# Kernel optimization log

Measured on AMD Instinct MI355X. Metric: run time of the kernel, lower is better.

The kernel has to match this reference:

```python
import jax, jax.numpy as jnp
import numpy as np
import math

B, N = 1, 768
C1, C2 = 384, 128
H, SQK, SV, PQK, PV, NC = 12, 16, 16, 4, 8, 384
EPS = 1e-8
SCALAR_W = math.sqrt(1.0 / (3.0 * SQK))           # sqrt(1/(num_logit_terms*scalar_variance))
POINT_W = math.sqrt(1.0 / (3.0 * (PQK * 9.0 / 2.0)))
W2D = math.sqrt(1.0 / 3.0)


def _quat_to_rot(q):
    # q: [..., 4] -> orthonormal rotation matrices [..., 3, 3]
    q = q / jnp.linalg.norm(q, axis=-1, keepdims=True)
    w, x, y, z = q[..., 0], q[..., 1], q[..., 2], q[..., 3]
    r0 = jnp.stack([1 - 2 * (y * y + z * z), 2 * (x * y - w * z), 2 * (x * z + w * y)], -1)
    r1 = jnp.stack([2 * (x * y + w * z), 1 - 2 * (x * x + z * z), 2 * (y * z - w * x)], -1)
    r2 = jnp.stack([2 * (x * z - w * y), 2 * (y * z + w * x), 1 - 2 * (x * x + y * y)], -1)
    return jnp.stack([r0, r1, r2], -2)


def setup_inputs() -> dict:
    key = jax.random.key(0)
    ks = jax.random.split(key, 12)

    def lin(k, o, i):
        kw, kb = jax.random.split(k)
        w = jax.random.normal(kw, (o, i), jnp.float32) / np.sqrt(i).astype(np.float32)
        b = jax.random.normal(kb, (o,), jnp.float32) * 0.01
        return w, b

    w_qs, b_qs = lin(ks[0], H * SQK, C1)
    w_kvs, b_kvs = lin(ks[1], H * (SV + SQK), C1)
    w_qp, b_qp = lin(ks[2], H * 3 * PQK, C1)
    w_kvp, b_kvp = lin(ks[3], H * 3 * (PQK + PV), C1)
    w_a2, b_a2 = lin(ks[4], H, C2)
    w_o, b_o = lin(ks[5], NC, H * (C2 + SV + 4 * PV))
    return {
        'inputs_1d': jax.random.normal(ks[6], (B, N, C1), jnp.float32),
        'inputs_2d': jax.random.normal(ks[7], (B, N, N, C2), jnp.float32),
        'mask': jnp.ones((B, N, 1), jnp.float32),
        'rotation': _quat_to_rot(jax.random.normal(ks[8], (B, N, 4), jnp.float32)),
        'translation': jax.random.normal(ks[9], (B, N, 3), jnp.float32) * 10.0,
        'w_q_scalar': w_qs, 'b_q_scalar': b_qs,
        'w_kv_scalar': w_kvs, 'b_kv_scalar': b_kvs,
        'w_q_point': w_qp, 'b_q_point': b_qp,
        'w_kv_point': w_kvp, 'b_kv_point': b_kvp,
        'tpw': jnp.ones((H,), jnp.float32),
        'w_attn2d': w_a2, 'b_attn2d': b_a2,
        'w_out': w_o, 'b_out': b_o,
    }


def ipa_forward(inputs_1d, inputs_2d, mask, rotation, translation,
                w_q_scalar, b_q_scalar, w_kv_scalar, b_kv_scalar,
                w_q_point, b_q_point, w_kv_point, b_kv_point,
                tpw, w_attn2d, b_attn2d, w_out, b_out):
    Bs, Ns, _ = inputs_1d.shape

    # scalar q/k/v
    q_scalar = (inputs_1d @ w_q_scalar.T + b_q_scalar).reshape(Bs, Ns, H, SQK)
    kv_scalar = (inputs_1d @ w_kv_scalar.T + b_kv_scalar).reshape(Bs, Ns, H, SQK + SV)
    k_scalar, v_scalar = kv_scalar[..., :SQK], kv_scalar[..., SQK:]

    # point q/k/v in local frame; split order is 3 coord chunks of size H*P
    qp = (inputs_1d @ w_q_point.T + b_q_point).reshape(Bs, Ns, 3, H * PQK)
    kvp = (inputs_1d @ w_kv_point.T + b_kv_point).reshape(Bs, Ns, 3, H * (PQK + PV))
    # to global frame: p_global = R @ p_local + t
    qg = jnp.einsum('bnij,bnjm->bnim', rotation, qp) + translation[..., None]
    kvg = jnp.einsum('bnij,bnjm->bnim', rotation, kvp) + translation[..., None]
    q_point = qg.reshape(Bs, Ns, 3, H, PQK).transpose(0, 3, 1, 4, 2)          # [B,H,N,Pqk,3]
    kv_point = kvg.reshape(Bs, Ns, 3, H, PQK + PV).transpose(0, 3, 1, 4, 2)    # [B,H,N,Pqk+Pv,3]
    k_point, v_point = kv_point[..., :PQK, :], kv_point[..., PQK:, :]

    # point-distance attention term: sum_{p,c} (q-k)^2 = |q|^2 + |k|^2 - 2 q.k
    pw = jax.nn.softplus(tpw) * POINT_W                                       # [H]
    qn = jnp.sum(q_point * q_point, axis=(-1, -2))                             # [B,H,N]
    kn = jnp.sum(k_point * k_point, axis=(-1, -2))
    qk = jnp.einsum('bhipc,bhjpc->bhij', q_point, k_point)
    dist2 = qn[..., :, None] + kn[..., None, :] - 2.0 * qk                     # [B,H,N,N]
    attn_qk_point = -0.5 * pw[None, :, None, None] * dist2

    # scalar attention term
    attn_qk_scalar = jnp.einsum('bihd,bjhd->bhij', SCALAR_W * q_scalar, k_scalar)

    # pair-bias term
    a2d = inputs_2d @ w_attn2d.T + b_attn2d                                    # [B,N,N,H]
    logits = attn_qk_scalar + attn_qk_point + W2D * a2d.transpose(0, 3, 1, 2)

    mask2d = mask * jnp.swapaxes(mask, -1, -2)                                 # [B,N,N]
    logits = logits - 1e5 * (1.0 - mask2d[:, None, :, :])
    attn = jax.nn.softmax(logits, axis=-1)                                     # [B,H,N,N]

    # scalar values
    result_scalar = jnp.einsum('bhij,bjhd->bihd', attn, v_scalar).reshape(Bs, Ns, H * SV)

    # point values (global), then back to local frame: p_local = R^T (p - t)
    rpg = jnp.einsum('bhij,bhjpc->bhipc', attn, v_point)                       # [B,H,N,Pv,3]
    rpg = rpg.transpose(0, 2, 4, 1, 3).reshape(Bs, Ns, 3, H * PV)              # [B,N,3,M]
    local = jnp.einsum('bnji,bnjm->bnim', rotation, rpg - translation[..., None])
    dist = jnp.sqrt(EPS + jnp.sum(local * local, axis=2))                      # [B,N,M]

    # attention over pair features
    r2d = jnp.einsum('bhij,bijc->bihc', attn, inputs_2d).reshape(Bs, Ns, H * C2)

    final_act = jnp.concatenate(
        [result_scalar, local[:, :, 0], local[:, :, 1], local[:, :, 2], dist, r2d], axis=-1)
    return final_act @ w_out.T + b_out


def reference(inputs_1d, inputs_2d, mask, rotation, translation,
              w_q_scalar, b_q_scalar, w_kv_scalar, b_kv_scalar,
              w_q_point, b_q_point, w_kv_point, b_kv_point,
              tpw, w_attn2d, b_attn2d, w_out, b_out):
    return ipa_forward(inputs_1d, inputs_2d, mask, rotation, translation,
                       w_q_scalar, b_q_scalar, w_kv_scalar, b_kv_scalar,
                       w_q_point, b_q_point, w_kv_point, b_kv_point,
                       tpw, w_attn2d, b_attn2d, w_out, b_out)
```

## Files before the change

### kernel.cpp

```cpp
#include <hip/hip_runtime.h>
#include <hip/hip_bf16.h>
#include <math.h>

#define NRES 768
#define C1 384
#define C2 128
#define NH 12

#define OFF_QS   0
#define OFF_KS   147456
#define OFF_VS   294912
#define OFF_QPT  442368
#define OFF_KPT  552960
#define OFF_VPT  663552
#define OFF_FA   884736
#define OFF_RAW  OFF_FA

__device__ __forceinline__ float dot4(float4 a, float4 b) {
    return fmaf(a.x, b.x, fmaf(a.y, b.y, fmaf(a.z, b.z, a.w * b.w)));
}

static constexpr float SCALAR_W = 0.14433756729740643f;
static constexpr float POINT_W  = 0.13608276348795434f;
static constexpr float W2D_W    = 0.57735026918962576f;

__device__ __forceinline__ void wsel(int o,
    const float* w_qs, const float* b_qs, const float* w_kvs, const float* b_kvs,
    const float* w_qp, const float* b_qp, const float* w_kvp, const float* b_kvp,
    const float** row, float* bias)
{
    if (o < 192)      { *row = w_qs  + (size_t)o * C1;         *bias = b_qs[o]; }
    else if (o < 576) { *row = w_kvs + (size_t)(o - 192) * C1; *bias = b_kvs[o - 192]; }
    else if (o < 720) { *row = w_qp  + (size_t)(o - 576) * C1; *bias = b_qp[o - 576]; }
    else              { *row = w_kvp + (size_t)(o - 720) * C1; *bias = b_kvp[o - 720]; }
}

__global__ __launch_bounds__(256) void k1_gemm(
    const float* __restrict__ in1d,
    const float* __restrict__ w_qs, const float* __restrict__ b_qs,
    const float* __restrict__ w_kvs, const float* __restrict__ b_kvs,
    const float* __restrict__ w_qp, const float* __restrict__ b_qp,
    const float* __restrict__ w_kvp, const float* __restrict__ b_kvp,
    float* __restrict__ ws)
{
    __shared__ __align__(16) float ASt[32][68];
    __shared__ __align__(16) float WSt[32][68];
    const int t = threadIdx.x;
    const int n0 = blockIdx.x * 64;
    const int o0 = blockIdx.y * 64;
    const int tx = t & 15, ty = t >> 4;
    float acc[4][4];
    #pragma unroll
    for (int r = 0; r < 4; ++r)
        #pragma unroll
        for (int c = 0; c < 4; ++c) acc[r][c] = 0.f;

    for (int k0 = 0; k0 < C1; k0 += 32) {
        __syncthreads();
        #pragma unroll
        for (int s = 0; s < 2; ++s) {
            int q = t + 256 * s;
            int row = q >> 3, kq = (q & 7) * 4;
            float4 a4 = *(const float4*)&in1d[(size_t)(n0 + row) * C1 + k0 + kq];
            ASt[kq + 0][row] = a4.x; ASt[kq + 1][row] = a4.y;
            ASt[kq + 2][row] = a4.z; ASt[kq + 3][row] = a4.w;
            const float* wr; float bb;
            wsel(o0 + row, w_qs, b_qs, w_kvs, b_kvs, w_qp, b_qp, w_kvp, b_kvp, &wr, &bb);
            float4 w4 = *(const float4*)&wr[k0 + kq];
            WSt[kq + 0][row] = w4.x; WSt[kq + 1][row] = w4.y;
            WSt[kq + 2][row] = w4.z; WSt[kq + 3][row] = w4.w;
        }
        __syncthreads();
        #pragma unroll
        for (int k = 0; k < 32; ++k) {
            float4 a4 = *(const float4*)&ASt[k][ty * 4];
            float4 w4 = *(const float4*)&WSt[k][tx * 4];
            float av[4] = {a4.x, a4.y, a4.z, a4.w};
            float wv[4] = {w4.x, w4.y, w4.z, w4.w};
            #pragma unroll
            for (int r = 0; r < 4; ++r)
                #pragma unroll
                for (int c = 0; c < 4; ++c)
                    acc[r][c] = fmaf(av[r], wv[c], acc[r][c]);
        }
    }
    float bias[4];
    #pragma unroll
    for (int c = 0; c < 4; ++c) {
        const float* dummy;
        wsel(o0 + tx * 4 + c, w_qs, b_qs, w_kvs, b_kvs, w_qp, b_qp, w_kvp, b_kvp, &dummy, &bias[c]);
    }
    float* raw = ws + OFF_RAW;
    #pragma unroll
    for (int r = 0; r < 4; ++r) {
        int n = n0 + ty * 4 + r;
        *(float4*)&raw[(size_t)n * 1152 + o0 + tx * 4] =
            make_float4(acc[r][0] + bias[0], acc[r][1] + bias[1],
                        acc[r][2] + bias[2], acc[r][3] + bias[3]);
    }
}

__global__ __launch_bounds__(256) void k1b_scatter(
    const float* __restrict__ rot, const float* __restrict__ trans,
    float* __restrict__ ws)
{
    __shared__ __align__(16) float rawS[1152];
    const int t = threadIdx.x;
    const int i = blockIdx.x;
    const float* raw = ws + OFF_RAW + (size_t)i * 1152;
    for (int q = t; q < 288; q += 256) *(float4*)&rawS[q * 4] = *(const float4*)&raw[q * 4];
    __syncthreads();
    float* qs  = ws + OFF_QS;  float* ks  = ws + OFF_KS;  float* vs  = ws + OFF_VS;
    float* qpt = ws + OFF_QPT; float* kpt = ws + OFF_KPT; float* vpt = ws + OFF_VPT;

    for (int o = t; o < 576; o += 256) {
        float v = rawS[o];
        if (o < 192) {
            qs[(size_t)i * 192 + o] = v * SCALAR_W;
        } else {
            int idx = o - 192, h = idx >> 5, d = idx & 31;
            if (d < 16) ks[(size_t)i * 192 + h * 16 + d] = v;
            else        vs[(size_t)i * 192 + h * 16 + (d - 16)] = v;
        }
    }
    if (t < 192) {
        int m = t;
        float x0, x1, x2;
        if (m < 48) { x0 = rawS[576 + m]; x1 = rawS[624 + m]; x2 = rawS[672 + m]; }
        else { int mm = m - 48; x0 = rawS[720 + mm]; x1 = rawS[864 + mm]; x2 = rawS[1008 + mm]; }
        float g[3];
        #pragma unroll
        for (int ii = 0; ii < 3; ++ii)
            g[ii] = rot[i * 9 + ii * 3 + 0] * x0 + rot[i * 9 + ii * 3 + 1] * x1 +
                    rot[i * 9 + ii * 3 + 2] * x2 + trans[i * 3 + ii];
        if (m < 48) {
            #pragma unroll
            for (int ii = 0; ii < 3; ++ii) qpt[(size_t)i * 144 + 3 * m + ii] = g[ii];
        } else {
            int mm = m - 48, h = mm / 12, pp = mm % 12;
            if (pp < 4) {
                #pragma unroll
                for (int ii = 0; ii < 3; ++ii) kpt[(size_t)i * 144 + h * 12 + pp * 3 + ii] = g[ii];
            } else {
                #pragma unroll
                for (int ii = 0; ii < 3; ++ii) vpt[(size_t)i * 288 + h * 24 + (pp - 4) * 3 + ii] = g[ii];
            }
        }
    }
}

#define TJ 256
__global__ __launch_bounds__(256) void k2_attn(
    const float* __restrict__ in2d,
    const float* __restrict__ mask,
    const float* __restrict__ rot, const float* __restrict__ trans,
    const float* __restrict__ tpw,
    const float* __restrict__ w2d, const float* __restrict__ b2d,
    float* __restrict__ ws)
{
    __shared__ __align__(16) float P[NH][264];
    __shared__ __align__(16) float tileS[64][128];
    __shared__ __align__(16) float qsS[192];
    __shared__ __align__(16) float qptS[144];
    __shared__ float qnS[NH], phS[NH], bbS[NH], mS[NH], lS[NH], aS[NH];
    __shared__ float rpgS[288];
    const int t = threadIdx.x;
    const int i = blockIdx.x;

    const float* qs  = ws + OFF_QS;  const float* ks  = ws + OFF_KS;  const float* vs = ws + OFF_VS;
    const float* qpt = ws + OFF_QPT; const float* kpt = ws + OFF_KPT; const float* vpt = ws + OFF_VPT;

    if (t < 48) *(float4*)&qsS[t * 4] = *(const float4*)&qs[(size_t)i * 192 + t * 4];
    else if (t >= 64 && t < 100) { int u = t - 64; *(float4*)&qptS[u * 4] = *(const float4*)&qpt[(size_t)i * 144 + u * 4]; }
    __syncthreads();
    if (t < NH) {
        float s = 0.f;
        #pragma unroll
        for (int e = 0; e < 12; ++e) { float x = qptS[t * 12 + e]; s += x * x; }
        qnS[t] = s;
        phS[t] = -0.5f * POINT_W * logf(1.f + __expf(tpw[t]));
        bbS[t] = W2D_W * b2d[t];
        mS[t] = -1e30f;
        lS[t] = 0.f;
    }
    __syncthreads();
    const float mi = mask[i];

    float ra[4] = {0.f, 0.f, 0.f, 0.f};
    float rb[4] = {0.f, 0.f, 0.f, 0.f};
    const bool isR2 = (t < 192);
    int h0 = 0, h1 = 0, c4 = 0, o0 = 0, vh = 0;
    const float* vbase = nullptr; int vstride = 0; bool vact = false;
    if (isR2) { h0 = (t >> 5) * 2; h1 = h0 + 1; c4 = t & 31; }
    else {
        int u = t - 192; o0 = u * 8; vact = (u < 60);
        if (vact) {
            if (o0 < 192) { vh = o0 >> 4; vbase = vs + o0; vstride = 192; }
            else { int q0 = o0 - 192; vh = q0 / 24; vbase = vpt + q0; vstride = 288; }
        }
    }

    for (int tile = 0; tile < 3; ++tile) {
        const int j0 = tile * TJ;
        __syncthreads();
        {
            const int j = j0 + t;
            float acc[NH];
            #pragma unroll
            for (int h = 0; h < NH; ++h) acc[h] = 0.f;
            const float* row = in2d + ((size_t)i * NRES + j) * C2;
            #pragma unroll 8
            for (int cc = 0; cc < 32; ++cc) {
                float4 v4 = *(const float4*)&row[cc * 4];
                #pragma unroll
                for (int h = 0; h < NH; ++h) {
                    float4 w4 = *(const float4*)&w2d[h * C2 + cc * 4];
                    acc[h] += dot4(v4, w4);
                }
            }
            const float msub = -100000.0f * (1.0f - mi * mask[j]);
            const float* ksr  = ks  + (size_t)j * 192;
            const float* kptr = kpt + (size_t)j * 144;
            #pragma unroll
            for (int h = 0; h < NH; ++h) {
                float sq = 0.f;
                #pragma unroll
                for (int d4 = 0; d4 < 4; ++d4) {
                    float4 q4 = *(const float4*)&qsS[h * 16 + d4 * 4];
                    float4 k4 = *(const float4*)&ksr[h * 16 + d4 * 4];
                    sq += dot4(q4, k4);
                }
                float qk = 0.f, kk = 0.f;
                #pragma unroll
                for (int e4 = 0; e4 < 3; ++e4) {
                    float4 qp4 = *(const float4*)&qptS[h * 12 + e4 * 4];
                    float4 kp4 = *(const float4*)&kptr[h * 12 + e4 * 4];
                    qk += dot4(qp4, kp4);
                    kk += dot4(kp4, kp4);
                }
                P[h][t] = sq + phS[h] * (qnS[h] + kk - 2.f * qk) + W2D_W * acc[h] + bbS[h] + msub;
            }
        }
        __syncthreads();
        {
            int wv = t >> 6, lane = t & 63;
            for (int h = wv * 3; h < wv * 3 + 3; ++h) {
                float v0 = P[h][lane], v1 = P[h][lane + 64], v2 = P[h][lane + 128], v3 = P[h][lane + 192];
                float mt = fmaxf(fmaxf(v0, v1), fmaxf(v2, v3));
                #pragma unroll
                for (int off = 32; off > 0; off >>= 1) mt = fmaxf(mt, __shfl_xor(mt, off));
                float mold = mS[h];
                float mnew = fmaxf(mold, mt);
                float e0 = __expf(v0 - mnew), e1 = __expf(v1 - mnew);
                float e2 = __expf(v2 - mnew), e3 = __expf(v3 - mnew);
                P[h][lane] = e0; P[h][lane + 64] = e1; P[h][lane + 128] = e2; P[h][lane + 192] = e3;
                float s = e0 + e1 + e2 + e3;
                #pragma unroll
                for (int off = 32; off > 0; off >>= 1) s += __shfl_xor(s, off);
                if (lane == 0) {
                    float a = __expf(mold - mnew);
                    aS[h] = a;
                    lS[h] = lS[h] * a + s;
                    mS[h] = mnew;
                }
            }
        }
        __syncthreads();
        if (isR2) {
            float a0 = aS[h0], a1 = aS[h1];
            #pragma unroll
            for (int k = 0; k < 4; ++k) { ra[k] *= a0; rb[k] *= a1; }
        } else if (vact) {
            float a = aS[vh];
            #pragma unroll
            for (int k = 0; k < 4; ++k) { ra[k] *= a; rb[k] *= a; }
        }
        for (int sub = 0; sub < 4; ++sub) {
            __syncthreads();
            #pragma unroll
            for (int s = 0; s < 8; ++s) {
                int q = t + 256 * s;
                int rr = q >> 5, cc = q & 31;
                *(float4*)&tileS[rr][cc * 4] =
                    *(const float4*)&in2d[((size_t)i * NRES + j0 + sub * 64 + rr) * C2 + cc * 4];
            }
            __syncthreads();
            if (isR2) {
                for (int jj = 0; jj < 64; jj += 4) {
                    int jt = sub * 64 + jj;
                    float4 p0 = *(const float4*)&P[h0][jt];
                    float4 p1 = *(const float4*)&P[h1][jt];
                    float w0[4] = {p0.x, p0.y, p0.z, p0.w};
                    float w1[4] = {p1.x, p1.y, p1.z, p1.w};
                    #pragma unroll
                    for (int k = 0; k < 4; ++k) {
                        float4 v4 = *(const float4*)&tileS[jj + k][c4 * 4];
                        ra[0] = fmaf(w0[k], v4.x, ra[0]); ra[1] = fmaf(w0[k], v4.y, ra[1]);
                        ra[2] = fmaf(w0[k], v4.z, ra[2]); ra[3] = fmaf(w0[k], v4.w, ra[3]);
                        rb[0] = fmaf(w1[k], v4.x, rb[0]); rb[1] = fmaf(w1[k], v4.y, rb[1]);
                        rb[2] = fmaf(w1[k], v4.z, rb[2]); rb[3] = fmaf(w1[k], v4.w, rb[3]);
                    }
                }
            } else if (vact) {
                for (int jj = 0; jj < 64; jj += 4) {
                    int jt = sub * 64 + jj;
                    int jg = j0 + jt;
                    float4 p = *(const float4*)&P[vh][jt];
                    float w[4] = {p.x, p.y, p.z, p.w};
                    #pragma unroll
                    for (int k = 0; k < 4; ++k) {
                        float4 va = *(const float4*)&vbase[(size_t)(jg + k) * vstride];
                        float4 vb = *(const float4*)&vbase[(size_t)(jg + k) * vstride + 4];
                        ra[0] = fmaf(w[k], va.x, ra[0]); ra[1] = fmaf(w[k], va.y, ra[1]);
                        ra[2] = fmaf(w[k], va.z, ra[2]); ra[3] = fmaf(w[k], va.w, ra[3]);
                        rb[0] = fmaf(w[k], vb.x, rb[0]); rb[1] = fmaf(w[k], vb.y, rb[1]);
                        rb[2] = fmaf(w[k], vb.z, rb[2]); rb[3] = fmaf(w[k], vb.w, rb[3]);
                    }
                }
            }
        }
    }
    float* fa = ws + OFF_FA + (size_t)i * 2112;
    if (isR2) {
        float n0v = 1.f / lS[h0], n1v = 1.f / lS[h1];
        *(float4*)&fa[576 + h0 * 128 + c4 * 4] = make_float4(ra[0] * n0v, ra[1] * n0v, ra[2] * n0v, ra[3] * n0v);
        *(float4*)&fa[576 + h1 * 128 + c4 * 4] = make_float4(rb[0] * n1v, rb[1] * n1v, rb[2] * n1v, rb[3] * n1v);
    } else if (vact) {
        float nv = 1.f / lS[vh];
        if (o0 < 192) {
            *(float4*)&fa[o0]     = make_float4(ra[0] * nv, ra[1] * nv, ra[2] * nv, ra[3] * nv);
            *(float4*)&fa[o0 + 4] = make_float4(rb[0] * nv, rb[1] * nv, rb[2] * nv, rb[3] * nv);
        } else {
            int q0 = o0 - 192;
            *(float4*)&rpgS[q0]     = make_float4(ra[0] * nv, ra[1] * nv, ra[2] * nv, ra[3] * nv);
            *(float4*)&rpgS[q0 + 4] = make_float4(rb[0] * nv, rb[1] * nv, rb[2] * nv, rb[3] * nv);
        }
    }
    __syncthreads();
    if (t < 96) {
        int h = t >> 3, p = t & 7;
        float rv[3];
        #pragma unroll
        for (int c = 0; c < 3; ++c) rv[c] = rpgS[h * 24 + p * 3 + c] - trans[i * 3 + c];
        float l0 = rot[i * 9 + 0] * rv[0] + rot[i * 9 + 3] * rv[1] + rot[i * 9 + 6] * rv[2];
        float l1 = rot[i * 9 + 1] * rv[0] + rot[i * 9 + 4] * rv[1] + rot[i * 9 + 7] * rv[2];
        float l2 = rot[i * 9 + 2] * rv[0] + rot[i * 9 + 5] * rv[1] + rot[i * 9 + 8] * rv[2];
        float dd = sqrtf(1e-8f + l0 * l0 + l1 * l1 + l2 * l2);
        fa[192 + t] = l0;
        fa[288 + t] = l1;
        fa[384 + t] = l2;
        fa[480 + t] = dd;
    }
}

__global__ __launch_bounds__(256) void k3_out(
    const float* __restrict__ w_out, const float* __restrict__ b_out,
    const float* __restrict__ ws, float* __restrict__ out)
{
    __shared__ __align__(16) float ASt[32][34];
    __shared__ __align__(16) float WSt[32][34];
    const int t = threadIdx.x;
    const int i0 = blockIdx.x * 32;
    const int o0 = blockIdx.y * 32;
    const float* fa = ws + OFF_FA;
    int tx = t & 15, ty = t >> 4;
    float acc00 = 0.f, acc01 = 0.f, acc10 = 0.f, acc11 = 0.f;
    int r = t >> 3, kq = (t & 7) * 4;

    for (int k0 = 0; k0 < 2112; k0 += 32) {
        __syncthreads();
        {
            float4 a4 = *(const float4*)&fa[(size_t)(i0 + r) * 2112 + k0 + kq];
            ASt[kq + 0][r] = a4.x; ASt[kq + 1][r] = a4.y; ASt[kq + 2][r] = a4.z; ASt[kq + 3][r] = a4.w;
            float4 w4 = *(const float4*)&w_out[(size_t)(o0 + r) * 2112 + k0 + kq];
            WSt[kq + 0][r] = w4.x; WSt[kq + 1][r] = w4.y; WSt[kq + 2][r] = w4.z; WSt[kq + 3][r] = w4.w;
        }
        __syncthreads();
        #pragma unroll
        for (int k = 0; k < 32; ++k) {
            float2 av = *(const float2*)&ASt[k][ty * 2];
            float2 wv = *(const float2*)&WSt[k][tx * 2];
            acc00 = fmaf(av.x, wv.x, acc00);
            acc01 = fmaf(av.x, wv.y, acc01);
            acc10 = fmaf(av.y, wv.x, acc10);
            acc11 = fmaf(av.y, wv.y, acc11);
        }
    }
    int oi = i0 + ty * 2, oo = o0 + tx * 2;
    out[(size_t)oi * 384 + oo]           = acc00 + b_out[oo];
    out[(size_t)oi * 384 + oo + 1]       = acc01 + b_out[oo + 1];
    out[(size_t)(oi + 1) * 384 + oo]     = acc10 + b_out[oo];
    out[(size_t)(oi + 1) * 384 + oo + 1] = acc11 + b_out[oo + 1];
}

extern "C" void kernel_launch(void* const* d_in, const int* in_sizes, int n_in,
                              void* d_out, int out_size, void* d_ws, size_t ws_size,
                              hipStream_t stream) {
    const float* in1d  = (const float*)d_in[0];
    const float* in2d  = (const float*)d_in[1];
    const float* mask  = (const float*)d_in[2];
    const float* rot   = (const float*)d_in[3];
    const float* trans = (const float*)d_in[4];
    const float* w_qs  = (const float*)d_in[5];
    const float* b_qs  = (const float*)d_in[6];
    const float* w_kvs = (const float*)d_in[7];
    const float* b_kvs = (const float*)d_in[8];
    const float* w_qp  = (const float*)d_in[9];
    const float* b_qp  = (const float*)d_in[10];
    const float* w_kvp = (const float*)d_in[11];
    const float* b_kvp = (const float*)d_in[12];
    const float* tpw   = (const float*)d_in[13];
    const float* w2d   = (const float*)d_in[14];
    const float* b2d   = (const float*)d_in[15];
    const float* w_out = (const float*)d_in[16];
    const float* b_out = (const float*)d_in[17];
    float* ws  = (float*)d_ws;
    float* out = (float*)d_out;

    hipLaunchKernelGGL(k1_gemm, dim3(12, 18), dim3(256), 0, stream,
                       in1d, w_qs, b_qs, w_kvs, b_kvs, w_qp, b_qp, w_kvp, b_kvp, ws);
    hipLaunchKernelGGL(k1b_scatter, dim3(768), dim3(256), 0, stream,
                       rot, trans, ws);
    hipLaunchKernelGGL(k2_attn, dim3(768), dim3(256), 0, stream,
                       in2d, mask, rot, trans, tpw, w2d, b2d, ws);
    hipLaunchKernelGGL(k3_out, dim3(24, 12), dim3(256), 0, stream,
                       w_out, b_out, ws, out);
}
```

Baseline: 703.8 us.

## Fuse logit and pair-feature passes over a register-prefetched 64-row tile

The attention kernel now reads each 64-row block of inputs_2d into shared memory once. It uses that tile both to project the 2D logits and to accumulate the attention-weighted pair features, instead of streaming the rows twice. Loads for the next tile go into registers while the current tile is being processed, and the online softmax now runs per 64-column step with each wave owning three heads. The tile row stride is padded to reduce LDS bank conflicts. In exchange, the kernel needs more registers for the prefetch buffer and does twelve softmax rescale and barrier rounds instead of three.

```diff
diff --git a/kernel.cpp b/kernel.cpp
--- a/kernel.cpp
+++ b/kernel.cpp
@@ -149,7 +149,7 @@
     }
 }
 
-#define TJ 256
+#define TSTR 132
 __global__ __launch_bounds__(256) void k2_attn(
     const float* __restrict__ in2d,
     const float* __restrict__ mask,
@@ -158,8 +158,8 @@
     const float* __restrict__ w2d, const float* __restrict__ b2d,
     float* __restrict__ ws)
 {
-    __shared__ __align__(16) float P[NH][264];
-    __shared__ __align__(16) float tileS[64][128];
+    __shared__ __align__(16) float tileS[64][TSTR];
+    __shared__ __align__(16) float P[NH][72];
     __shared__ __align__(16) float qsS[192];
     __shared__ __align__(16) float qptS[144];
     __shared__ float qnS[NH], phS[NH], bbS[NH], mS[NH], lS[NH], aS[NH];
@@ -170,6 +170,14 @@
     const float* qs  = ws + OFF_QS;  const float* ks  = ws + OFF_KS;  const float* vs = ws + OFF_VS;
     const float* qpt = ws + OFF_QPT; const float* kpt = ws + OFF_KPT; const float* vpt = ws + OFF_VPT;
 
+    float4 pf[8];
+    #pragma unroll
+    for (int u = 0; u < 8; ++u) {
+        int q = t + 256 * u;
+        int rr = q >> 5, cc = q & 31;
+        pf[u] = *(const float4*)&in2d[((size_t)i * NRES + rr) * C2 + cc * 4];
+    }
+
     if (t < 48) *(float4*)&qsS[t * 4] = *(const float4*)&qs[(size_t)i * 192 + t * 4];
     else if (t >= 64 && t < 100) { int u = t - 64; *(float4*)&qptS[u * 4] = *(const float4*)&qpt[(size_t)i * 144 + u * 4]; }
     __syncthreads();
@@ -183,8 +191,20 @@
         mS[t] = -1e30f;
         lS[t] = 0.f;
     }
+    #pragma unroll
+    for (int u = 0; u < 8; ++u) {
+        int q = t + 256 * u;
+        int rr = q >> 5, cc = q & 31;
+        *(float4*)&tileS[rr][cc * 4] = pf[u];
+    }
     __syncthreads();
+
     const float mi = mask[i];
+    const int jl = t & 63;
+    const int hbase = (t >> 6) * 3;
+    const float* w2d0 = w2d + (size_t)(hbase + 0) * C2;
+    const float* w2d1 = w2d + (size_t)(hbase + 1) * C2;
+    const float* w2d2 = w2d + (size_t)(hbase + 2) * C2;
 
     float ra[4] = {0.f, 0.f, 0.f, 0.f};
     float rb[4] = {0.f, 0.f, 0.f, 0.f};
@@ -200,29 +220,34 @@
         }
     }
 
-    for (int tile = 0; tile < 3; ++tile) {
-        const int j0 = tile * TJ;
-        __syncthreads();
+    for (int s = 0; s < 12; ++s) {
+        const int j0 = s * 64;
+        if (s < 11) {
+            #pragma unroll
+            for (int u = 0; u < 8; ++u) {
+                int q = t + 256 * u;
+                int rr = q >> 5, cc = q & 31;
+                pf[u] = *(const float4*)&in2d[((size_t)i * NRES + j0 + 64 + rr) * C2 + cc * 4];
+            }
+        }
         {
-            const int j = j0 + t;
-            float acc[NH];
-            #pragma unroll
-            for (int h = 0; h < NH; ++h) acc[h] = 0.f;
-            const float* row = in2d + ((size_t)i * NRES + j) * C2;
+            const int jg = j0 + jl;
+            float a0 = 0.f, a1 = 0.f, a2 = 0.f;
+            const float* trow = &tileS[jl][0];
             #pragma unroll 8
             for (int cc = 0; cc < 32; ++cc) {
-                float4 v4 = *(const float4*)&row[cc * 4];
-                #pragma unroll
-                for (int h = 0; h < NH; ++h) {
-                    float4 w4 = *(const float4*)&w2d[h * C2 + cc * 4];
-                    acc[h] += dot4(v4, w4);
-                }
-            }
-            const float msub = -100000.0f * (1.0f - mi * mask[j]);
-            const float* ksr  = ks  + (size_t)j * 192;
-            const float* kptr = kpt + (size_t)j * 144;
-            #pragma unroll
-            for (int h = 0; h < NH; ++h) {
+                float4 v4 = *(const float4*)&trow[cc * 4];
+                a0 += dot4(v4, *(const float4*)&w2d0[cc * 4]);
+                a1 += dot4(v4, *(const float4*)&w2d1[cc * 4]);
+                a2 += dot4(v4, *(const float4*)&w2d2[cc * 4]);
+            }
+            const float msub = -100000.0f * (1.0f - mi * mask[jg]);
+            const float* ksr  = ks  + (size_t)jg * 192;
+            const float* kptr = kpt + (size_t)jg * 144;
+            float av[3] = {a0, a1, a2};
+            #pragma unroll
+            for (int g = 0; g < 3; ++g) {
+                const int h = hbase + g;
                 float sq = 0.f;
                 #pragma unroll
                 for (int d4 = 0; d4 < 4; ++d4) {
@@ -238,29 +263,28 @@
                     qk += dot4(qp4, kp4);
                     kk += dot4(kp4, kp4);
                 }
-                P[h][t] = sq + phS[h] * (qnS[h] + kk - 2.f * qk) + W2D_W * acc[h] + bbS[h] + msub;
-            }
-        }
-        __syncthreads();
+                P[h][jl] = sq + phS[h] * (qnS[h] + kk - 2.f * qk) + W2D_W * av[g] + bbS[h] + msub;
+            }
+        }
         {
-            int wv = t >> 6, lane = t & 63;
-            for (int h = wv * 3; h < wv * 3 + 3; ++h) {
-                float v0 = P[h][lane], v1 = P[h][lane + 64], v2 = P[h][lane + 128], v3 = P[h][lane + 192];
-                float mt = fmaxf(fmaxf(v0, v1), fmaxf(v2, v3));
+            #pragma unroll
+            for (int g = 0; g < 3; ++g) {
+                const int h = hbase + g;
+                float v = P[h][jl];
+                float mt = v;
                 #pragma unroll
                 for (int off = 32; off > 0; off >>= 1) mt = fmaxf(mt, __shfl_xor(mt, off));
                 float mold = mS[h];
                 float mnew = fmaxf(mold, mt);
-                float e0 = __expf(v0 - mnew), e1 = __expf(v1 - mnew);
-                float e2 = __expf(v2 - mnew), e3 = __expf(v3 - mnew);
-                P[h][lane] = e0; P[h][lane + 64] = e1; P[h][lane + 128] = e2; P[h][lane + 192] = e3;
-                float s = e0 + e1 + e2 + e3;
-                #pragma unroll
-                for (int off = 32; off > 0; off >>= 1) s += __shfl_xor(s, off);
-                if (lane == 0) {
+                float e = __expf(v - mnew);
+                P[h][jl] = e;
+                float ss = e;
+                #pragma unroll
+                for (int off = 32; off > 0; off >>= 1) ss += __shfl_xor(ss, off);
+                if (jl == 0) {
                     float a = __expf(mold - mnew);
                     aS[h] = a;
-                    lS[h] = lS[h] * a + s;
+                    lS[h] = lS[h] * a + ss;
                     mS[h] = mnew;
                 }
             }
@@ -270,54 +294,48 @@
             float a0 = aS[h0], a1 = aS[h1];
             #pragma unroll
             for (int k = 0; k < 4; ++k) { ra[k] *= a0; rb[k] *= a1; }
+            for (int jj = 0; jj < 64; jj += 4) {
+                float4 p0 = *(const float4*)&P[h0][jj];
+                float4 p1 = *(const float4*)&P[h1][jj];
+                float w0[4] = {p0.x, p0.y, p0.z, p0.w};
+                float w1[4] = {p1.x, p1.y, p1.z, p1.w};
+                #pragma unroll
+                for (int k = 0; k < 4; ++k) {
+                    float4 v4 = *(const float4*)&tileS[jj + k][c4 * 4];
+                    ra[0] = fmaf(w0[k], v4.x, ra[0]); ra[1] = fmaf(w0[k], v4.y, ra[1]);
+                    ra[2] = fmaf(w0[k], v4.z, ra[2]); ra[3] = fmaf(w0[k], v4.w, ra[3]);
+                    rb[0] = fmaf(w1[k], v4.x, rb[0]); rb[1] = fmaf(w1[k], v4.y, rb[1]);
+                    rb[2] = fmaf(w1[k], v4.z, rb[2]); rb[3] = fmaf(w1[k], v4.w, rb[3]);
+                }
+            }
         } else if (vact) {
             float a = aS[vh];
             #pragma unroll
             for (int k = 0; k < 4; ++k) { ra[k] *= a; rb[k] *= a; }
-        }
-        for (int sub = 0; sub < 4; ++sub) {
+            for (int jj = 0; jj < 64; jj += 4) {
+                const int jgg = j0 + jj;
+                float4 p = *(const float4*)&P[vh][jj];
+                float w[4] = {p.x, p.y, p.z, p.w};
+                #pragma unroll
+                for (int k = 0; k < 4; ++k) {
+                    float4 va4 = *(const float4*)&vbase[(size_t)(jgg + k) * vstride];
+                    float4 vb4 = *(const float4*)&vbase[(size_t)(jgg + k) * vstride + 4];
+                    ra[0] = fmaf(w[k], va4.x, ra[0]); ra[1] = fmaf(w[k], va4.y, ra[1]);
+                    ra[2] = fmaf(w[k], va4.z, ra[2]); ra[3] = fmaf(w[k], va4.w, ra[3]);
+                    rb[0] = fmaf(w[k], vb4.x, rb[0]); rb[1] = fmaf(w[k], vb4.y, rb[1]);
+                    rb[2] = fmaf(w[k], vb4.z, rb[2]); rb[3] = fmaf(w[k], vb4.w, rb[3]);
+                }
+            }
+        }
+        if (s < 11) {
             __syncthreads();
             #pragma unroll
-            for (int s = 0; s < 8; ++s) {
-                int q = t + 256 * s;
+            for (int u = 0; u < 8; ++u) {
+                int q = t + 256 * u;
                 int rr = q >> 5, cc = q & 31;
-                *(float4*)&tileS[rr][cc * 4] =
-                    *(const float4*)&in2d[((size_t)i * NRES + j0 + sub * 64 + rr) * C2 + cc * 4];
+                *(float4*)&tileS[rr][cc * 4] = pf[u];
             }
             __syncthreads();
-            if (isR2) {
-                for (int jj = 0; jj < 64; jj += 4) {
-                    int jt = sub * 64 + jj;
-                    float4 p0 = *(const float4*)&P[h0][jt];
-                    float4 p1 = *(const float4*)&P[h1][jt];
-                    float w0[4] = {p0.x, p0.y, p0.z, p0.w};
-                    float w1[4] = {p1.x, p1.y, p1.z, p1.w};
-                    #pragma unroll
-                    for (int k = 0; k < 4; ++k) {
-                        float4 v4 = *(const float4*)&tileS[jj + k][c4 * 4];
-                        ra[0] = fmaf(w0[k], v4.x, ra[0]); ra[1] = fmaf(w0[k], v4.y, ra[1]);
-                        ra[2] = fmaf(w0[k], v4.z, ra[2]); ra[3] = fmaf(w0[k], v4.w, ra[3]);
-                        rb[0] = fmaf(w1[k], v4.x, rb[0]); rb[1] = fmaf(w1[k], v4.y, rb[1]);
-                        rb[2] = fmaf(w1[k], v4.z, rb[2]); rb[3] = fmaf(w1[k], v4.w, rb[3]);
-                    }
-                }
-            } else if (vact) {
-                for (int jj = 0; jj < 64; jj += 4) {
-                    int jt = sub * 64 + jj;
-                    int jg = j0 + jt;
-                    float4 p = *(const float4*)&P[vh][jt];
-                    float w[4] = {p.x, p.y, p.z, p.w};
-                    #pragma unroll
-                    for (int k = 0; k < 4; ++k) {
-                        float4 va = *(const float4*)&vbase[(size_t)(jg + k) * vstride];
-                        float4 vb = *(const float4*)&vbase[(size_t)(jg + k) * vstride + 4];
-                        ra[0] = fmaf(w[k], va.x, ra[0]); ra[1] = fmaf(w[k], va.y, ra[1]);
-                        ra[2] = fmaf(w[k], va.z, ra[2]); ra[3] = fmaf(w[k], va.w, ra[3]);
-                        rb[0] = fmaf(w[k], vb.x, rb[0]); rb[1] = fmaf(w[k], vb.y, rb[1]);
-                        rb[2] = fmaf(w[k], vb.z, rb[2]); rb[3] = fmaf(w[k], vb.w, rb[3]);
-                    }
-                }
-            }
         }
     }
     float* fa = ws + OFF_FA + (size_t)i * 2112;
```

Result: slower. 1.025 ms (+45.7%).

## Split attention kernel across head groups and read pair tiles directly from global

Applied to the files above, without the earlier changes.

The attention kernel now launches two blocks per residue, each handling six heads. This halves per-block shared memory by dropping the 64x128 pair-feature tile and shrinking the logits buffer, and adds an occupancy hint to the launch bounds. The weighted sum over pair features now reads in2d straight from global memory, with each thread owning one head instead of two, so there are fewer block barriers. The trade-off is that the 2D input is read twice per residue (once per head group), and the 2D projection is split between the two blocks, so the large in2d tensor sees extra global or cache traffic.

```diff
diff --git a/kernel.cpp b/kernel.cpp
--- a/kernel.cpp
+++ b/kernel.cpp
@@ -6,6 +6,7 @@
 #define C1 384
 #define C2 128
 #define NH 12
+#define HB 6
 
 #define OFF_QS   0
 #define OFF_KS   147456
@@ -149,8 +150,7 @@
     }
 }
 
-#define TJ 256
-__global__ __launch_bounds__(256) void k2_attn(
+__global__ __launch_bounds__(256, 6) void k2_attn(
     const float* __restrict__ in2d,
     const float* __restrict__ mask,
     const float* __restrict__ rot, const float* __restrict__ trans,
@@ -158,14 +158,15 @@
     const float* __restrict__ w2d, const float* __restrict__ b2d,
     float* __restrict__ ws)
 {
-    __shared__ __align__(16) float P[NH][264];
-    __shared__ __align__(16) float tileS[64][128];
+    __shared__ __align__(16) float P[HB][264];
     __shared__ __align__(16) float qsS[192];
     __shared__ __align__(16) float qptS[144];
-    __shared__ float qnS[NH], phS[NH], bbS[NH], mS[NH], lS[NH], aS[NH];
-    __shared__ float rpgS[288];
-    const int t = threadIdx.x;
-    const int i = blockIdx.x;
+    __shared__ float qnS[HB], phS[HB], bbS[HB], mS[HB], lS[HB], aS[HB];
+    __shared__ float rpgS[144];
+    const int t  = threadIdx.x;
+    const int hg = blockIdx.x;
+    const int i  = blockIdx.y;
+    const int h0 = hg * HB;
 
     const float* qs  = ws + OFF_QS;  const float* ks  = ws + OFF_KS;  const float* vs = ws + OFF_VS;
     const float* qpt = ws + OFF_QPT; const float* kpt = ws + OFF_KPT; const float* vpt = ws + OFF_VPT;
@@ -173,13 +174,14 @@
     if (t < 48) *(float4*)&qsS[t * 4] = *(const float4*)&qs[(size_t)i * 192 + t * 4];
     else if (t >= 64 && t < 100) { int u = t - 64; *(float4*)&qptS[u * 4] = *(const float4*)&qpt[(size_t)i * 144 + u * 4]; }
     __syncthreads();
-    if (t < NH) {
+    if (t < HB) {
+        int h = h0 + t;
         float s = 0.f;
         #pragma unroll
-        for (int e = 0; e < 12; ++e) { float x = qptS[t * 12 + e]; s += x * x; }
+        for (int e = 0; e < 12; ++e) { float x = qptS[h * 12 + e]; s += x * x; }
         qnS[t] = s;
-        phS[t] = -0.5f * POINT_W * logf(1.f + __expf(tpw[t]));
-        bbS[t] = W2D_W * b2d[t];
+        phS[t] = -0.5f * POINT_W * logf(1.f + __expf(tpw[h]));
+        bbS[t] = W2D_W * b2d[h];
         mS[t] = -1e30f;
         lS[t] = 0.f;
     }
@@ -189,167 +191,148 @@
     float ra[4] = {0.f, 0.f, 0.f, 0.f};
     float rb[4] = {0.f, 0.f, 0.f, 0.f};
     const bool isR2 = (t < 192);
-    int h0 = 0, h1 = 0, c4 = 0, o0 = 0, vh = 0;
+    int lh = 0, c4 = 0, o0 = 0, q0 = 0, vh = 0;
     const float* vbase = nullptr; int vstride = 0; bool vact = false;
-    if (isR2) { h0 = (t >> 5) * 2; h1 = h0 + 1; c4 = t & 31; }
+    if (isR2) { lh = t >> 5; c4 = t & 31; }
     else {
-        int u = t - 192; o0 = u * 8; vact = (u < 60);
+        int u = t - 192; vact = (u < 30); o0 = u * 8;
         if (vact) {
-            if (o0 < 192) { vh = o0 >> 4; vbase = vs + o0; vstride = 192; }
-            else { int q0 = o0 - 192; vh = q0 / 24; vbase = vpt + q0; vstride = 288; }
+            if (u < 12) { vh = u >> 1; vbase = vs + (size_t)h0 * 16 + o0; vstride = 192; }
+            else { q0 = o0 - 96; vh = q0 / 24; vbase = vpt + (size_t)h0 * 24 + q0; vstride = 288; }
         }
     }
 
     for (int tile = 0; tile < 3; ++tile) {
-        const int j0 = tile * TJ;
+        const int j0 = tile * 256;
         __syncthreads();
         {
             const int j = j0 + t;
-            float acc[NH];
-            #pragma unroll
-            for (int h = 0; h < NH; ++h) acc[h] = 0.f;
-            const float* row = in2d + ((size_t)i * NRES + j) * C2;
+            float acc[HB];
+            #pragma unroll
+            for (int g = 0; g < HB; ++g) acc[g] = 0.f;
+            const float* row   = in2d + ((size_t)i * NRES + j) * C2;
+            const float* wbase = w2d + (size_t)h0 * C2;
             #pragma unroll 8
             for (int cc = 0; cc < 32; ++cc) {
                 float4 v4 = *(const float4*)&row[cc * 4];
                 #pragma unroll
-                for (int h = 0; h < NH; ++h) {
-                    float4 w4 = *(const float4*)&w2d[h * C2 + cc * 4];
-                    acc[h] += dot4(v4, w4);
+                for (int g = 0; g < HB; ++g) {
+                    float4 w4 = *(const float4*)&wbase[g * C2 + cc * 4];
+                    acc[g] += dot4(v4, w4);
                 }
             }
             const float msub = -100000.0f * (1.0f - mi * mask[j]);
-            const float* ksr  = ks  + (size_t)j * 192;
-            const float* kptr = kpt + (size_t)j * 144;
-            #pragma unroll
-            for (int h = 0; h < NH; ++h) {
+            const float* ksr  = ks  + (size_t)j * 192 + h0 * 16;
+            const float* kptr = kpt + (size_t)j * 144 + h0 * 12;
+            #pragma unroll
+            for (int g = 0; g < HB; ++g) {
                 float sq = 0.f;
                 #pragma unroll
                 for (int d4 = 0; d4 < 4; ++d4) {
-                    float4 q4 = *(const float4*)&qsS[h * 16 + d4 * 4];
-                    float4 k4 = *(const float4*)&ksr[h * 16 + d4 * 4];
+                    float4 q4 = *(const float4*)&qsS[(h0 + g) * 16 + d4 * 4];
+                    float4 k4 = *(const float4*)&ksr[g * 16 + d4 * 4];
                     sq += dot4(q4, k4);
                 }
                 float qk = 0.f, kk = 0.f;
                 #pragma unroll
                 for (int e4 = 0; e4 < 3; ++e4) {
-                    float4 qp4 = *(const float4*)&qptS[h * 12 + e4 * 4];
-                    float4 kp4 = *(const float4*)&kptr[h * 12 + e4 * 4];
+                    float4 qp4 = *(const float4*)&qptS[(h0 + g) * 12 + e4 * 4];
+                    float4 kp4 = *(const float4*)&kptr[g * 12 + e4 * 4];
                     qk += dot4(qp4, kp4);
                     kk += dot4(kp4, kp4);
                 }
-                P[h][t] = sq + phS[h] * (qnS[h] + kk - 2.f * qk) + W2D_W * acc[h] + bbS[h] + msub;
+                P[g][t] = sq + phS[g] * (qnS[g] + kk - 2.f * qk) + W2D_W * acc[g] + bbS[g] + msub;
             }
         }
         __syncthreads();
         {
             int wv = t >> 6, lane = t & 63;
-            for (int h = wv * 3; h < wv * 3 + 3; ++h) {
-                float v0 = P[h][lane], v1 = P[h][lane + 64], v2 = P[h][lane + 128], v3 = P[h][lane + 192];
+            for (int g = wv; g < HB; g += 4) {
+                float v0 = P[g][lane], v1 = P[g][lane + 64], v2 = P[g][lane + 128], v3 = P[g][lane + 192];
                 float mt = fmaxf(fmaxf(v0, v1), fmaxf(v2, v3));
                 #pragma unroll
                 for (int off = 32; off > 0; off >>= 1) mt = fmaxf(mt, __shfl_xor(mt, off));
-                float mold = mS[h];
+                float mold = mS[g];
                 float mnew = fmaxf(mold, mt);
                 float e0 = __expf(v0 - mnew), e1 = __expf(v1 - mnew);
                 float e2 = __expf(v2 - mnew), e3 = __expf(v3 - mnew);
-                P[h][lane] = e0; P[h][lane + 64] = e1; P[h][lane + 128] = e2; P[h][lane + 192] = e3;
+                P[g][lane] = e0; P[g][lane + 64] = e1; P[g][lane + 128] = e2; P[g][lane + 192] = e3;
                 float s = e0 + e1 + e2 + e3;
                 #pragma unroll
                 for (int off = 32; off > 0; off >>= 1) s += __shfl_xor(s, off);
                 if (lane == 0) {
                     float a = __expf(mold - mnew);
-                    aS[h] = a;
-                    lS[h] = lS[h] * a + s;
-                    mS[h] = mnew;
+                    aS[g] = a;
+                    lS[g] = lS[g] * a + s;
+                    mS[g] = mnew;
                 }
             }
         }
         __syncthreads();
         if (isR2) {
-            float a0 = aS[h0], a1 = aS[h1];
-            #pragma unroll
-            for (int k = 0; k < 4; ++k) { ra[k] *= a0; rb[k] *= a1; }
+            float a = aS[lh];
+            #pragma unroll
+            for (int k = 0; k < 4; ++k) ra[k] *= a;
+            const float* r2base = in2d + ((size_t)i * NRES + j0) * C2 + c4 * 4;
+            for (int jj = 0; jj < 256; jj += 4) {
+                float4 p4 = *(const float4*)&P[lh][jj];
+                float w[4] = {p4.x, p4.y, p4.z, p4.w};
+                #pragma unroll
+                for (int k = 0; k < 4; ++k) {
+                    float4 v4 = *(const float4*)&r2base[(size_t)(jj + k) * C2];
+                    ra[0] = fmaf(w[k], v4.x, ra[0]); ra[1] = fmaf(w[k], v4.y, ra[1]);
+                    ra[2] = fmaf(w[k], v4.z, ra[2]); ra[3] = fmaf(w[k], v4.w, ra[3]);
+                }
+            }
         } else if (vact) {
             float a = aS[vh];
             #pragma unroll
             for (int k = 0; k < 4; ++k) { ra[k] *= a; rb[k] *= a; }
-        }
-        for (int sub = 0; sub < 4; ++sub) {
-            __syncthreads();
-            #pragma unroll
-            for (int s = 0; s < 8; ++s) {
-                int q = t + 256 * s;
-                int rr = q >> 5, cc = q & 31;
-                *(float4*)&tileS[rr][cc * 4] =
-                    *(const float4*)&in2d[((size_t)i * NRES + j0 + sub * 64 + rr) * C2 + cc * 4];
-            }
-            __syncthreads();
-            if (isR2) {
-                for (int jj = 0; jj < 64; jj += 4) {
-                    int jt = sub * 64 + jj;
-                    float4 p0 = *(const float4*)&P[h0][jt];
-                    float4 p1 = *(const float4*)&P[h1][jt];
-                    float w0[4] = {p0.x, p0.y, p0.z, p0.w};
-                    float w1[4] = {p1.x, p1.y, p1.z, p1.w};
-                    #pragma unroll
-                    for (int k = 0; k < 4; ++k) {
-                        float4 v4 = *(const float4*)&tileS[jj + k][c4 * 4];
-                        ra[0] = fmaf(w0[k], v4.x, ra[0]); ra[1] = fmaf(w0[k], v4.y, ra[1]);
-                        ra[2] = fmaf(w0[k], v4.z, ra[2]); ra[3] = fmaf(w0[k], v4.w, ra[3]);
-                        rb[0] = fmaf(w1[k], v4.x, rb[0]); rb[1] = fmaf(w1[k], v4.y, rb[1]);
-                        rb[2] = fmaf(w1[k], v4.z, rb[2]); rb[3] = fmaf(w1[k], v4.w, rb[3]);
-                    }
-                }
-            } else if (vact) {
-                for (int jj = 0; jj < 64; jj += 4) {
-                    int jt = sub * 64 + jj;
-                    int jg = j0 + jt;
-                    float4 p = *(const float4*)&P[vh][jt];
-                    float w[4] = {p.x, p.y, p.z, p.w};
-                    #pragma unroll
-                    for (int k = 0; k < 4; ++k) {
-                        float4 va = *(const float4*)&vbase[(size_t)(jg + k) * vstride];
-                        float4 vb = *(const float4*)&vbase[(size_t)(jg + k) * vstride + 4];
-                        ra[0] = fmaf(w[k], va.x, ra[0]); ra[1] = fmaf(w[k], va.y, ra[1]);
-                        ra[2] = fmaf(w[k], va.z, ra[2]); ra[3] = fmaf(w[k], va.w, ra[3]);
-                        rb[0] = fmaf(w[k], vb.x, rb[0]); rb[1] = fmaf(w[k], vb.y, rb[1]);
-                        rb[2] = fmaf(w[k], vb.z, rb[2]); rb[3] = fmaf(w[k], vb.w, rb[3]);
-                    }
+            for (int jj = 0; jj < 256; jj += 4) {
+                const int jg = j0 + jj;
+                float4 p = *(const float4*)&P[vh][jj];
+                float w[4] = {p.x, p.y, p.z, p.w};
+                #pragma unroll
+                for (int k = 0; k < 4; ++k) {
+                    float4 va4 = *(const float4*)&vbase[(size_t)(jg + k) * vstride];
+                    float4 vb4 = *(const float4*)&vbase[(size_t)(jg + k) * vstride + 4];
+                    ra[0] = fmaf(w[k], va4.x, ra[0]); ra[1] = fmaf(w[k], va4.y, ra[1]);
+                    ra[2] = fmaf(w[k], va4.z, ra[2]); ra[3] = fmaf(w[k], va4.w, ra[3]);
+                    rb[0] = fmaf(w[k], vb4.x, rb[0]); rb[1] = fmaf(w[k], vb4.y, rb[1]);
+                    rb[2] = fmaf(w[k], vb4.z, rb[2]); rb[3] = fmaf(w[k], vb4.w, rb[3]);
                 }
             }
         }
     }
     float* fa = ws + OFF_FA + (size_t)i * 2112;
     if (isR2) {
-        float n0v = 1.f / lS[h0], n1v = 1.f / lS[h1];
-        *(float4*)&fa[576 + h0 * 128 + c4 * 4] = make_float4(ra[0] * n0v, ra[1] * n0v, ra[2] * n0v, ra[3] * n0v);
-        *(float4*)&fa[576 + h1 * 128 + c4 * 4] = make_float4(rb[0] * n1v, rb[1] * n1v, rb[2] * n1v, rb[3] * n1v);
+        float nv = 1.f / lS[lh];
+        *(float4*)&fa[576 + (h0 + lh) * 128 + c4 * 4] = make_float4(ra[0] * nv, ra[1] * nv, ra[2] * nv, ra[3] * nv);
     } else if (vact) {
         float nv = 1.f / lS[vh];
-        if (o0 < 192) {
-            *(float4*)&fa[o0]     = make_float4(ra[0] * nv, ra[1] * nv, ra[2] * nv, ra[3] * nv);
-            *(float4*)&fa[o0 + 4] = make_float4(rb[0] * nv, rb[1] * nv, rb[2] * nv, rb[3] * nv);
+        if (o0 < 96) {
+            *(float4*)&fa[h0 * 16 + o0]     = make_float4(ra[0] * nv, ra[1] * nv, ra[2] * nv, ra[3] * nv);
+            *(float4*)&fa[h0 * 16 + o0 + 4] = make_float4(rb[0] * nv, rb[1] * nv, rb[2] * nv, rb[3] * nv);
         } else {
-            int q0 = o0 - 192;
             *(float4*)&rpgS[q0]     = make_float4(ra[0] * nv, ra[1] * nv, ra[2] * nv, ra[3] * nv);
             *(float4*)&rpgS[q0 + 4] = make_float4(rb[0] * nv, rb[1] * nv, rb[2] * nv, rb[3] * nv);
         }
     }
     __syncthreads();
-    if (t < 96) {
-        int h = t >> 3, p = t & 7;
+    if (t < 48) {
+        int g = t >> 3, p = t & 7;
+        int gh = h0 + g;
         float rv[3];
         #pragma unroll
-        for (int c = 0; c < 3; ++c) rv[c] = rpgS[h * 24 + p * 3 + c] - trans[i * 3 + c];
+        for (int c = 0; c < 3; ++c) rv[c] = rpgS[g * 24 + p * 3 + c] - trans[i * 3 + c];
         float l0 = rot[i * 9 + 0] * rv[0] + rot[i * 9 + 3] * rv[1] + rot[i * 9 + 6] * rv[2];
         float l1 = rot[i * 9 + 1] * rv[0] + rot[i * 9 + 4] * rv[1] + rot[i * 9 + 7] * rv[2];
         float l2 = rot[i * 9 + 2] * rv[0] + rot[i * 9 + 5] * rv[1] + rot[i * 9 + 8] * rv[2];
         float dd = sqrtf(1e-8f + l0 * l0 + l1 * l1 + l2 * l2);
-        fa[192 + t] = l0;
-        fa[288 + t] = l1;
-        fa[384 + t] = l2;
-        fa[480 + t] = dd;
+        fa[192 + gh * 8 + p] = l0;
+        fa[288 + gh * 8 + p] = l1;
+        fa[384 + gh * 8 + p] = l2;
+        fa[480 + gh * 8 + p] = dd;
     }
 }
 
@@ -421,7 +404,7 @@
                        in1d, w_qs, b_qs, w_kvs, b_kvs, w_qp, b_qp, w_kvp, b_kvp, ws);
     hipLaunchKernelGGL(k1b_scatter, dim3(768), dim3(256), 0, stream,
                        rot, trans, ws);
-    hipLaunchKernelGGL(k2_attn, dim3(768), dim3(256), 0, stream,
+    hipLaunchKernelGGL(k2_attn, dim3(2, 768), dim3(256), 0, stream,
                        in2d, mask, rot, trans, tpw, w2d, b2d, ws);
     hipLaunchKernelGGL(k3_out, dim3(24, 12), dim3(256), 0, stream,
                        w_out, b_out, ws, out);
```

New measurement: 871.1 us. +23.8%, slower.

## Use 4x4 register tiles with split-K atomics in output GEMM; halve attention tile

Applied to the files above, without the earlier changes.

The output projection GEMM now uses 64x64 block tiles with a 4x4 register tile per thread and splits K into three chunks. Partial sums are combined with atomicAdd into an output zeroed by an added memset, and only the first chunk adds the bias. The pair-feature staging tile in the attention kernel is halved to 32 rows, which lowers shared memory use and may allow more resident blocks, at the cost of twice as many syncs. Atomics make the summation order nondeterministic, and the extra memset adds a launch.

```diff
diff --git a/kernel.cpp b/kernel.cpp
--- a/kernel.cpp
+++ b/kernel.cpp
@@ -159,7 +159,7 @@
     float* __restrict__ ws)
 {
     __shared__ __align__(16) float P[NH][264];
-    __shared__ __align__(16) float tileS[64][128];
+    __shared__ __align__(16) float tileS[32][128];
     __shared__ __align__(16) float qsS[192];
     __shared__ __align__(16) float qptS[144];
     __shared__ float qnS[NH], phS[NH], bbS[NH], mS[NH], lS[NH], aS[NH];
@@ -275,19 +275,19 @@
             #pragma unroll
             for (int k = 0; k < 4; ++k) { ra[k] *= a; rb[k] *= a; }
         }
-        for (int sub = 0; sub < 4; ++sub) {
+        for (int sub = 0; sub < 8; ++sub) {
             __syncthreads();
             #pragma unroll
-            for (int s = 0; s < 8; ++s) {
+            for (int s = 0; s < 4; ++s) {
                 int q = t + 256 * s;
                 int rr = q >> 5, cc = q & 31;
                 *(float4*)&tileS[rr][cc * 4] =
-                    *(const float4*)&in2d[((size_t)i * NRES + j0 + sub * 64 + rr) * C2 + cc * 4];
+                    *(const float4*)&in2d[((size_t)i * NRES + j0 + sub * 32 + rr) * C2 + cc * 4];
             }
             __syncthreads();
             if (isR2) {
-                for (int jj = 0; jj < 64; jj += 4) {
-                    int jt = sub * 64 + jj;
+                for (int jj = 0; jj < 32; jj += 4) {
+                    int jt = sub * 32 + jj;
                     float4 p0 = *(const float4*)&P[h0][jt];
                     float4 p1 = *(const float4*)&P[h1][jt];
                     float w0[4] = {p0.x, p0.y, p0.z, p0.w};
@@ -302,8 +302,8 @@
                     }
                 }
             } else if (vact) {
-                for (int jj = 0; jj < 64; jj += 4) {
-                    int jt = sub * 64 + jj;
+                for (int jj = 0; jj < 32; jj += 4) {
+                    int jt = sub * 32 + jj;
                     int jg = j0 + jt;
                     float4 p = *(const float4*)&P[vh][jt];
                     float w[4] = {p.x, p.y, p.z, p.w};
@@ -357,40 +357,61 @@
     const float* __restrict__ w_out, const float* __restrict__ b_out,
     const float* __restrict__ ws, float* __restrict__ out)
 {
-    __shared__ __align__(16) float ASt[32][34];
-    __shared__ __align__(16) float WSt[32][34];
+    __shared__ __align__(16) float ASt[32][68];
+    __shared__ __align__(16) float WSt[32][68];
     const int t = threadIdx.x;
-    const int i0 = blockIdx.x * 32;
-    const int o0 = blockIdx.y * 32;
+    const int i0 = blockIdx.x * 64;
+    const int o0 = blockIdx.y * 64;
+    const int kz = blockIdx.z;
+    const int kbase = kz * 704;
     const float* fa = ws + OFF_FA;
-    int tx = t & 15, ty = t >> 4;
-    float acc00 = 0.f, acc01 = 0.f, acc10 = 0.f, acc11 = 0.f;
-    int r = t >> 3, kq = (t & 7) * 4;
-
-    for (int k0 = 0; k0 < 2112; k0 += 32) {
-        __syncthreads();
-        {
-            float4 a4 = *(const float4*)&fa[(size_t)(i0 + r) * 2112 + k0 + kq];
-            ASt[kq + 0][r] = a4.x; ASt[kq + 1][r] = a4.y; ASt[kq + 2][r] = a4.z; ASt[kq + 3][r] = a4.w;
-            float4 w4 = *(const float4*)&w_out[(size_t)(o0 + r) * 2112 + k0 + kq];
-            WSt[kq + 0][r] = w4.x; WSt[kq + 1][r] = w4.y; WSt[kq + 2][r] = w4.z; WSt[kq + 3][r] = w4.w;
+    const int tx = t & 15, ty = t >> 4;
+    float acc[4][4];
+    #pragma unroll
+    for (int r = 0; r < 4; ++r)
+        #pragma unroll
+        for (int c = 0; c < 4; ++c) acc[r][c] = 0.f;
+
+    for (int k0 = 0; k0 < 704; k0 += 32) {
+        __syncthreads();
+        #pragma unroll
+        for (int s = 0; s < 2; ++s) {
+            int q = t + 256 * s;
+            int row = q >> 3, kq = (q & 7) * 4;
+            float4 a4 = *(const float4*)&fa[(size_t)(i0 + row) * 2112 + kbase + k0 + kq];
+            ASt[kq + 0][row] = a4.x; ASt[kq + 1][row] = a4.y;
+            ASt[kq + 2][row] = a4.z; ASt[kq + 3][row] = a4.w;
+            float4 w4 = *(const float4*)&w_out[(size_t)(o0 + row) * 2112 + kbase + k0 + kq];
+            WSt[kq + 0][row] = w4.x; WSt[kq + 1][row] = w4.y;
+            WSt[kq + 2][row] = w4.z; WSt[kq + 3][row] = w4.w;
         }
         __syncthreads();
         #pragma unroll
         for (int k = 0; k < 32; ++k) {
-            float2 av = *(const float2*)&ASt[k][ty * 2];
-            float2 wv = *(const float2*)&WSt[k][tx * 2];
-            acc00 = fmaf(av.x, wv.x, acc00);
-            acc01 = fmaf(av.x, wv.y, acc01);
-            acc10 = fmaf(av.y, wv.x, acc10);
-            acc11 = fmaf(av.y, wv.y, acc11);
-        }
-    }
-    int oi = i0 + ty * 2, oo = o0 + tx * 2;
-    out[(size_t)oi * 384 + oo]           = acc00 + b_out[oo];
-    out[(size_t)oi * 384 + oo + 1]       = acc01 + b_out[oo + 1];
-    out[(size_t)(oi + 1) * 384 + oo]     = acc10 + b_out[oo];
-    out[(size_t)(oi + 1) * 384 + oo + 1] = acc11 + b_out[oo + 1];
+            float4 a4 = *(const float4*)&ASt[k][ty * 4];
+            float4 w4 = *(const float4*)&WSt[k][tx * 4];
+            float av[4] = {a4.x, a4.y, a4.z, a4.w};
+            float wv[4] = {w4.x, w4.y, w4.z, w4.w};
+            #pragma unroll
+            for (int r = 0; r < 4; ++r)
+                #pragma unroll
+                for (int c = 0; c < 4; ++c)
+                    acc[r][c] = fmaf(av[r], wv[c], acc[r][c]);
+        }
+    }
+    float bias[4] = {0.f, 0.f, 0.f, 0.f};
+    if (kz == 0) {
+        #pragma unroll
+        for (int c = 0; c < 4; ++c) bias[c] = b_out[o0 + tx * 4 + c];
+    }
+    #pragma unroll
+    for (int r = 0; r < 4; ++r) {
+        int oi = i0 + ty * 4 + r;
+        #pragma unroll
+        for (int c = 0; c < 4; ++c) {
+            atomicAdd(&out[(size_t)oi * 384 + o0 + tx * 4 + c], acc[r][c] + bias[c]);
+        }
+    }
 }
 
 extern "C" void kernel_launch(void* const* d_in, const int* in_sizes, int n_in,
@@ -423,6 +444,7 @@
                        rot, trans, ws);
     hipLaunchKernelGGL(k2_attn, dim3(768), dim3(256), 0, stream,
                        in2d, mask, rot, trans, tpw, w2d, b2d, ws);
-    hipLaunchKernelGGL(k3_out, dim3(24, 12), dim3(256), 0, stream,
+    hipMemsetAsync(d_out, 0, out_size, stream);
+    hipLaunchKernelGGL(k3_out, dim3(12, 6, 3), dim3(256), 0, stream,
                        w_out, b_out, ws, out);
 }
```

Result: slower. 800.1 us (+13.7%).
